# Optimization experiments

Measured on AMD Instinct MI355X. Metric: run time of the kernel, lower is better.

Reference implementation:

```python
import jax, jax.numpy as jnp
import numpy as np


def hadamard(D):
    # Sylvester Hadamard: H[i,j] = (-1)^popcount(i & j), normalized by sqrt(D)
    x = np.arange(D)[:, None] & np.arange(D)[None, :]
    par = np.zeros_like(x)
    for _ in range(int(np.log2(D)) + 1):
        par ^= x & 1
        x >>= 1
    return ((1.0 - 2.0 * par) / np.sqrt(D)).astype(np.float32)


def setup_inputs() -> dict:
    key = jax.random.key(0)
    ks = jax.random.split(key, 6)
    K, M, D, T = 4, 32, 2048, 128
    z = jax.random.normal(ks[0], (K, M, D, T), dtype=jnp.float32)
    d1 = jax.random.normal(ks[1], (D, 1), dtype=jnp.float32)
    d2 = jax.random.normal(ks[2], (D, 1), dtype=jnp.float32)
    d3 = jax.random.normal(ks[3], (D, 1), dtype=jnp.float32)
    b = jax.random.normal(ks[4], (D, 1), dtype=jnp.float32)
    sldj = jax.random.normal(ks[5], (K * M,), dtype=jnp.float32)
    return {"z": z, "d1": d1, "d2": d2, "d3": d3, "b": b,
            "sum_log_det_jacobians": sldj}


def reference(z, d1, d2, d3, b, sum_log_det_jacobians):
    K, M, D, T = z.shape
    H = jnp.asarray(hadamard(D), dtype=z.dtype)
    # A = H @ D3 @ H @ D2 @ H @ D1
    #   H @ diag(d)  == H * d.T (scale columns)
    #   diag(d) @ X  == d * X   (scale rows)
    A = H @ (d3 * (H @ (d2 * (H * d1[:, 0][None, :]))))
    # apply: tensordot(A, z, [[1],[2]]) then transpose to (K,M,D,T), add bias
    z_out = jnp.einsum('de,kmet->kmdt', A, z) + b[None, None, :, :]
    # log|det A| = sum_i log|d1_i| + log|d2_i| + log|d3_i|  (H is orthogonal)
    log_det_A = (jnp.sum(jnp.log(jnp.abs(d1)))
                 + jnp.sum(jnp.log(jnp.abs(d2)))
                 + jnp.sum(jnp.log(jnp.abs(d3))))
    sldj = sum_log_det_jacobians + log_det_A * jnp.ones((K * M,), dtype=z.dtype)
    return z_out, sldj
```

## Files before the change

### kernel.cpp

```cpp
#include <hip/hip_runtime.h>
#include <math.h>

#define D_DIM 2048
#define T_DIM 128
#define TT 16

__device__ __forceinline__ int sw1(int x) { return x ^ ((x >> 5) & 1); }
__device__ __forceinline__ int sw2(int x) { return x ^ ((x >> 4) & 1); }

#define BFLY(MM)                                              \
    _Pragma("unroll")                                         \
    for (int i_ = 0; i_ < 64; ++i_) {                         \
        if ((i_ & (MM)) == 0) {                               \
            float a_ = v[i_], b_ = v[i_ | (MM)];              \
            v[i_] = a_ + b_;                                  \
            v[i_ | (MM)] = a_ - b_;                           \
        }                                                     \
    }

__global__ __launch_bounds__(512, 2)
void fwht_apply_kernel(const float* __restrict__ z,
                       const float* __restrict__ d1,
                       const float* __restrict__ d2,
                       const float* __restrict__ d3,
                       const float* __restrict__ bvec,
                       const float* __restrict__ sldj_in,
                       float* __restrict__ out) {
    __shared__ float lds[1024 * TT];
    const int tid = threadIdx.x;

    if (blockIdx.x == 1024) {
        float acc = 0.0f;
        for (int i = tid; i < D_DIM; i += 512)
            acc += logf(fabsf(d1[i])) + logf(fabsf(d2[i])) + logf(fabsf(d3[i]));
        lds[tid] = acc;
        __syncthreads();
        #pragma unroll
        for (int sft = 256; sft > 0; sft >>= 1) {
            if (tid < sft) lds[tid] += lds[tid + sft];
            __syncthreads();
        }
        if (tid < 128)
            out[(size_t)4 * 32 * 2048 * 128 + tid] = sldj_in[tid] + lds[0];
        return;
    }

    const int r   = tid >> 4;
    const int tt  = tid & 15;
    const int bid = blockIdx.x;
    const int km  = bid >> 3;
    const int t0  = (bid & 7) << 4;
    const float s = 0.022097086912079608f;

    const float* zslab = z + ((size_t)km << 18) + t0;
    const int wid  = tid >> 6;
    const int lane = tid & 63;
    const int q    = lane >> 2;
    const int c    = lane & 3;

    float v[64];

    #pragma unroll
    for (int h = 0; h < 2; ++h) {
        #pragma unroll
        for (int i = 0; i < 8; ++i) {
            const int n = (wid << 3) | i;
            const int e = (n << 5) | (h << 4) | q;
            float4 tmp = *(const float4*)(zslab + (size_t)e * T_DIM + (c << 2));
            ((float4*)lds)[(n << 6) + (q << 2) + c] = tmp;
        }
        __syncthreads();
        if (((r >> 4) & 1) == h) {
            #pragma unroll
            for (int j = 0; j < 64; ++j) {
                const int e = (j << 5) | r;
                v[j] = lds[(((r & 15) | (j << 4)) << 4) + tt] * (d1[e] * s);
            }
        }
        __syncthreads();
    }

    BFLY(1) BFLY(2) BFLY(4) BFLY(8) BFLY(16) BFLY(32)

    #pragma unroll
    for (int j = 0; j < 32; ++j)
        lds[sw1((j << 5) | r) * TT + tt] = v[j];
    __syncthreads();
    #pragma unroll
    for (int j = 0; j < 32; ++j)
        v[j] = lds[sw1(j | (r << 5)) * TT + tt];
    __syncthreads();
    #pragma unroll
    for (int j = 32; j < 64; ++j)
        lds[sw1(((j & 31) << 5) | r) * TT + tt] = v[j];
    __syncthreads();
    #pragma unroll
    for (int j = 32; j < 64; ++j)
        v[j] = lds[sw1((j & 31) | (r << 5)) * TT + tt];
    __syncthreads();

    BFLY(1) BFLY(2) BFLY(4) BFLY(8) BFLY(16)
    {
        const float4* q0 = (const float4*)(d2 + (r << 5));
        const float4* q1 = (const float4*)(d2 + 1024 + (r << 5));
        #pragma unroll
        for (int qq = 0; qq < 8; ++qq) {
            float4 a = q0[qq];
            v[4*qq+0] *= a.x * s; v[4*qq+1] *= a.y * s;
            v[4*qq+2] *= a.z * s; v[4*qq+3] *= a.w * s;
            float4 cc = q1[qq];
            v[32+4*qq+0] *= cc.x * s; v[32+4*qq+1] *= cc.y * s;
            v[32+4*qq+2] *= cc.z * s; v[32+4*qq+3] *= cc.w * s;
        }
    }
    BFLY(1) BFLY(2) BFLY(4) BFLY(8) BFLY(16) BFLY(32)

    #pragma unroll
    for (int j = 0; j < 64; j += 2)
        lds[sw2(((j >> 1) & 15) | (r << 4) | ((j >> 5) << 9)) * TT + tt] = v[j];
    __syncthreads();
    #pragma unroll
    for (int j = 0; j < 64; j += 2)
        v[j] = lds[sw2((((j >> 1) & 31) << 4) | (r & 15) | ((r >> 4) << 9)) * TT + tt];
    __syncthreads();
    #pragma unroll
    for (int j = 1; j < 64; j += 2)
        lds[sw2(((j >> 1) & 15) | (r << 4) | ((j >> 5) << 9)) * TT + tt] = v[j];
    __syncthreads();
    #pragma unroll
    for (int j = 1; j < 64; j += 2)
        v[j] = lds[sw2((((j >> 1) & 31) << 4) | (r & 15) | ((r >> 4) << 9)) * TT + tt];
    __syncthreads();

    BFLY(2) BFLY(4) BFLY(8) BFLY(16) BFLY(32)
    {
        const int eRest = ((r & 15) << 1) | ((r >> 4) << 10);
        #pragma unroll
        for (int m = 0; m < 32; ++m) {
            float2 a = *(const float2*)(d3 + ((m << 5) | eRest));
            v[2*m]   *= a.x * s;
            v[2*m+1] *= a.y * s;
        }
    }
    BFLY(2) BFLY(4) BFLY(8) BFLY(16) BFLY(32) BFLY(1)

    #pragma unroll
    for (int j = 0; j < 64; j += 2)
        lds[sw2((((j >> 1) & 31) << 4) | (r & 15) | ((r >> 4) << 9)) * TT + tt] = v[j];
    __syncthreads();
    #pragma unroll
    for (int j = 0; j < 64; j += 2)
        v[j] = lds[sw2(((j >> 1) & 15) | (r << 4) | ((j >> 5) << 9)) * TT + tt];
    __syncthreads();
    #pragma unroll
    for (int j = 1; j < 64; j += 2)
        lds[sw2((((j >> 1) & 31) << 4) | (r & 15) | ((r >> 4) << 9)) * TT + tt] = v[j];
    __syncthreads();
    #pragma unroll
    for (int j = 1; j < 64; j += 2)
        v[j] = lds[sw2(((j >> 1) & 15) | (r << 4) | ((j >> 5) << 9)) * TT + tt];

    BFLY(2) BFLY(4) BFLY(8) BFLY(16) BFLY(32)

    float* ob = out + ((size_t)km << 18) + t0 + tt;
    {
        const float4* q0 = (const float4*)(bvec + (r << 5));
        const float4* q1 = (const float4*)(bvec + 1024 + (r << 5));
        #pragma unroll
        for (int qq = 0; qq < 8; ++qq) {
            float4 a = q0[qq];
            const int e0 = (r << 5) + 4*qq;
            ob[(size_t)(e0+0) * T_DIM] = v[4*qq+0] + a.x;
            ob[(size_t)(e0+1) * T_DIM] = v[4*qq+1] + a.y;
            ob[(size_t)(e0+2) * T_DIM] = v[4*qq+2] + a.z;
            ob[(size_t)(e0+3) * T_DIM] = v[4*qq+3] + a.w;
            float4 cc = q1[qq];
            const int e1 = 1024 + (r << 5) + 4*qq;
            ob[(size_t)(e1+0) * T_DIM] = v[32+4*qq+0] + cc.x;
            ob[(size_t)(e1+1) * T_DIM] = v[32+4*qq+1] + cc.y;
            ob[(size_t)(e1+2) * T_DIM] = v[32+4*qq+2] + cc.z;
            ob[(size_t)(e1+3) * T_DIM] = v[32+4*qq+3] + cc.w;
        }
    }
}

extern "C" void kernel_launch(void* const* d_in, const int* in_sizes, int n_in,
                              void* d_out, int out_size, void* d_ws, size_t ws_size,
                              hipStream_t stream) {
    const float* z    = (const float*)d_in[0];
    const float* d1   = (const float*)d_in[1];
    const float* d2   = (const float*)d_in[2];
    const float* d3   = (const float*)d_in[3];
    const float* bvec = (const float*)d_in[4];
    const float* sldj = (const float*)d_in[5];
    float* out = (float*)d_out;

    fwht_apply_kernel<<<1025, 512, 0, stream>>>(z, d1, d2, d3, bvec, sldj, out);
}
```

Measured before the change: 303.4 us.

## Halve block to 256 threads with 8-column tiles and two passes per block

New measurement: 835.5 us. +175.4%, slower.

```diff
diff --git a/kernel.cpp b/kernel.cpp
--- a/kernel.cpp
+++ b/kernel.cpp
@@ -3,10 +3,10 @@
 
 #define D_DIM 2048
 #define T_DIM 128
-#define TT 16
-
-__device__ __forceinline__ int sw1(int x) { return x ^ ((x >> 5) & 1); }
-__device__ __forceinline__ int sw2(int x) { return x ^ ((x >> 4) & 1); }
+#define TT 8
+
+__device__ __forceinline__ int sw1(int x) { return x ^ ((x >> 5) & 3); }
+__device__ __forceinline__ int sw2(int x) { return x ^ ((x >> 4) & 3); }
 
 #define BFLY(MM)                                              \
     _Pragma("unroll")                                         \
@@ -18,7 +18,7 @@
         }                                                     \
     }
 
-__global__ __launch_bounds__(512, 2)
+__global__ __launch_bounds__(256, 4)
 void fwht_apply_kernel(const float* __restrict__ z,
                        const float* __restrict__ d1,
                        const float* __restrict__ d2,
@@ -31,12 +31,12 @@
 
     if (blockIdx.x == 1024) {
         float acc = 0.0f;
-        for (int i = tid; i < D_DIM; i += 512)
+        for (int i = tid; i < D_DIM; i += 256)
             acc += logf(fabsf(d1[i])) + logf(fabsf(d2[i])) + logf(fabsf(d3[i]));
         lds[tid] = acc;
         __syncthreads();
         #pragma unroll
-        for (int sft = 256; sft > 0; sft >>= 1) {
+        for (int sft = 128; sft > 0; sft >>= 1) {
             if (tid < sft) lds[tid] += lds[tid + sft];
             __syncthreads();
         }
@@ -45,141 +45,147 @@
         return;
     }
 
-    const int r   = tid >> 4;
-    const int tt  = tid & 15;
+    const int r   = tid >> 3;
+    const int tt  = tid & 7;
     const int bid = blockIdx.x;
-    const int km  = bid >> 3;
-    const int t0  = (bid & 7) << 4;
+    const int km  = bid & 127;
+    const int p0  = bid >> 7;
     const float s = 0.022097086912079608f;
 
-    const float* zslab = z + ((size_t)km << 18) + t0;
     const int wid  = tid >> 6;
     const int lane = tid & 63;
-    const int q    = lane >> 2;
-    const int c    = lane & 3;
-
-    float v[64];
-
-    #pragma unroll
-    for (int h = 0; h < 2; ++h) {
-        #pragma unroll
-        for (int i = 0; i < 8; ++i) {
-            const int n = (wid << 3) | i;
-            const int e = (n << 5) | (h << 4) | q;
-            float4 tmp = *(const float4*)(zslab + (size_t)e * T_DIM + (c << 2));
-            ((float4*)lds)[(n << 6) + (q << 2) + c] = tmp;
-        }
-        __syncthreads();
-        if (((r >> 4) & 1) == h) {
-            #pragma unroll
-            for (int j = 0; j < 64; ++j) {
-                const int e = (j << 5) | r;
-                v[j] = lds[(((r & 15) | (j << 4)) << 4) + tt] * (d1[e] * s);
-            }
-        }
-        __syncthreads();
-    }
-
-    BFLY(1) BFLY(2) BFLY(4) BFLY(8) BFLY(16) BFLY(32)
-
-    #pragma unroll
-    for (int j = 0; j < 32; ++j)
-        lds[sw1((j << 5) | r) * TT + tt] = v[j];
-    __syncthreads();
-    #pragma unroll
-    for (int j = 0; j < 32; ++j)
-        v[j] = lds[sw1(j | (r << 5)) * TT + tt];
-    __syncthreads();
-    #pragma unroll
-    for (int j = 32; j < 64; ++j)
-        lds[sw1(((j & 31) << 5) | r) * TT + tt] = v[j];
-    __syncthreads();
-    #pragma unroll
-    for (int j = 32; j < 64; ++j)
-        v[j] = lds[sw1((j & 31) | (r << 5)) * TT + tt];
-    __syncthreads();
-
-    BFLY(1) BFLY(2) BFLY(4) BFLY(8) BFLY(16)
-    {
-        const float4* q0 = (const float4*)(d2 + (r << 5));
-        const float4* q1 = (const float4*)(d2 + 1024 + (r << 5));
-        #pragma unroll
-        for (int qq = 0; qq < 8; ++qq) {
-            float4 a = q0[qq];
-            v[4*qq+0] *= a.x * s; v[4*qq+1] *= a.y * s;
-            v[4*qq+2] *= a.z * s; v[4*qq+3] *= a.w * s;
-            float4 cc = q1[qq];
-            v[32+4*qq+0] *= cc.x * s; v[32+4*qq+1] *= cc.y * s;
-            v[32+4*qq+2] *= cc.z * s; v[32+4*qq+3] *= cc.w * s;
-        }
-    }
-    BFLY(1) BFLY(2) BFLY(4) BFLY(8) BFLY(16) BFLY(32)
-
-    #pragma unroll
-    for (int j = 0; j < 64; j += 2)
-        lds[sw2(((j >> 1) & 15) | (r << 4) | ((j >> 5) << 9)) * TT + tt] = v[j];
-    __syncthreads();
-    #pragma unroll
-    for (int j = 0; j < 64; j += 2)
-        v[j] = lds[sw2((((j >> 1) & 31) << 4) | (r & 15) | ((r >> 4) << 9)) * TT + tt];
-    __syncthreads();
-    #pragma unroll
-    for (int j = 1; j < 64; j += 2)
-        lds[sw2(((j >> 1) & 15) | (r << 4) | ((j >> 5) << 9)) * TT + tt] = v[j];
-    __syncthreads();
-    #pragma unroll
-    for (int j = 1; j < 64; j += 2)
-        v[j] = lds[sw2((((j >> 1) & 31) << 4) | (r & 15) | ((r >> 4) << 9)) * TT + tt];
-    __syncthreads();
-
-    BFLY(2) BFLY(4) BFLY(8) BFLY(16) BFLY(32)
-    {
-        const int eRest = ((r & 15) << 1) | ((r >> 4) << 10);
-        #pragma unroll
-        for (int m = 0; m < 32; ++m) {
-            float2 a = *(const float2*)(d3 + ((m << 5) | eRest));
-            v[2*m]   *= a.x * s;
-            v[2*m+1] *= a.y * s;
-        }
-    }
-    BFLY(2) BFLY(4) BFLY(8) BFLY(16) BFLY(32) BFLY(1)
-
-    #pragma unroll
-    for (int j = 0; j < 64; j += 2)
-        lds[sw2((((j >> 1) & 31) << 4) | (r & 15) | ((r >> 4) << 9)) * TT + tt] = v[j];
-    __syncthreads();
-    #pragma unroll
-    for (int j = 0; j < 64; j += 2)
-        v[j] = lds[sw2(((j >> 1) & 15) | (r << 4) | ((j >> 5) << 9)) * TT + tt];
-    __syncthreads();
-    #pragma unroll
-    for (int j = 1; j < 64; j += 2)
-        lds[sw2((((j >> 1) & 31) << 4) | (r & 15) | ((r >> 4) << 9)) * TT + tt] = v[j];
-    __syncthreads();
-    #pragma unroll
-    for (int j = 1; j < 64; j += 2)
-        v[j] = lds[sw2(((j >> 1) & 15) | (r << 4) | ((j >> 5) << 9)) * TT + tt];
-
-    BFLY(2) BFLY(4) BFLY(8) BFLY(16) BFLY(32)
-
-    float* ob = out + ((size_t)km << 18) + t0 + tt;
-    {
-        const float4* q0 = (const float4*)(bvec + (r << 5));
-        const float4* q1 = (const float4*)(bvec + 1024 + (r << 5));
-        #pragma unroll
-        for (int qq = 0; qq < 8; ++qq) {
-            float4 a = q0[qq];
-            const int e0 = (r << 5) + 4*qq;
-            ob[(size_t)(e0+0) * T_DIM] = v[4*qq+0] + a.x;
-            ob[(size_t)(e0+1) * T_DIM] = v[4*qq+1] + a.y;
-            ob[(size_t)(e0+2) * T_DIM] = v[4*qq+2] + a.z;
-            ob[(size_t)(e0+3) * T_DIM] = v[4*qq+3] + a.w;
-            float4 cc = q1[qq];
-            const int e1 = 1024 + (r << 5) + 4*qq;
-            ob[(size_t)(e1+0) * T_DIM] = v[32+4*qq+0] + cc.x;
-            ob[(size_t)(e1+1) * T_DIM] = v[32+4*qq+1] + cc.y;
-            ob[(size_t)(e1+2) * T_DIM] = v[32+4*qq+2] + cc.z;
-            ob[(size_t)(e1+3) * T_DIM] = v[32+4*qq+3] + cc.w;
+    const int q    = (lane >> 1) & 15;
+    const int c    = lane & 1;
+    const int nl   = lane >> 5;
+
+    #pragma unroll 1
+    for (int p = 0; p < 2; ++p) {
+        const int t0 = (p0 << 4) | (p << 3);
+        const float* zslab = z + ((size_t)km << 18) + t0;
+        float v[64];
+        __syncthreads();
+
+        #pragma unroll
+        for (int h = 0; h < 2; ++h) {
+            #pragma unroll
+            for (int i = 0; i < 8; ++i) {
+                const int n = (wid << 4) | (i << 1) | nl;
+                const int e = (n << 5) | (h << 4) | q;
+                float4 tmp = *(const float4*)(zslab + (size_t)e * T_DIM + (c << 2));
+                ((float4*)lds)[(n << 5) + (q << 1) + c] = tmp;
+            }
+            __syncthreads();
+            if (((r >> 4) & 1) == h) {
+                #pragma unroll
+                for (int j = 0; j < 64; ++j) {
+                    const int e = (j << 5) | r;
+                    v[j] = lds[(j << 7) + ((r & 15) << 3) + tt] * (d1[e] * s);
+                }
+            }
+            __syncthreads();
+        }
+
+        BFLY(1) BFLY(2) BFLY(4) BFLY(8) BFLY(16) BFLY(32)
+
+        #pragma unroll
+        for (int j = 0; j < 32; ++j)
+            lds[(sw1((j << 5) | r) << 3) + tt] = v[j];
+        __syncthreads();
+        #pragma unroll
+        for (int j = 0; j < 32; ++j)
+            v[j] = lds[(sw1(j | (r << 5)) << 3) + tt];
+        __syncthreads();
+        #pragma unroll
+        for (int j = 32; j < 64; ++j)
+            lds[(sw1(((j & 31) << 5) | r) << 3) + tt] = v[j];
+        __syncthreads();
+        #pragma unroll
+        for (int j = 32; j < 64; ++j)
+            v[j] = lds[(sw1((j & 31) | (r << 5)) << 3) + tt];
+        __syncthreads();
+
+        BFLY(1) BFLY(2) BFLY(4) BFLY(8) BFLY(16)
+        {
+            const float4* q0 = (const float4*)(d2 + (r << 5));
+            const float4* q1 = (const float4*)(d2 + 1024 + (r << 5));
+            #pragma unroll
+            for (int qq = 0; qq < 8; ++qq) {
+                float4 a = q0[qq];
+                v[4*qq+0] *= a.x * s; v[4*qq+1] *= a.y * s;
+                v[4*qq+2] *= a.z * s; v[4*qq+3] *= a.w * s;
+                float4 cc = q1[qq];
+                v[32+4*qq+0] *= cc.x * s; v[32+4*qq+1] *= cc.y * s;
+                v[32+4*qq+2] *= cc.z * s; v[32+4*qq+3] *= cc.w * s;
+            }
+        }
+        BFLY(1) BFLY(2) BFLY(4) BFLY(8) BFLY(16) BFLY(32)
+
+        #pragma unroll
+        for (int j = 0; j < 64; j += 2)
+            lds[(sw2(((j >> 1) & 15) | (r << 4) | ((j >> 5) << 9)) << 3) + tt] = v[j];
+        __syncthreads();
+        #pragma unroll
+        for (int j = 0; j < 64; j += 2)
+            v[j] = lds[(sw2((((j >> 1) & 31) << 4) | (r & 15) | ((r >> 4) << 9)) << 3) + tt];
+        __syncthreads();
+        #pragma unroll
+        for (int j = 1; j < 64; j += 2)
+            lds[(sw2(((j >> 1) & 15) | (r << 4) | ((j >> 5) << 9)) << 3) + tt] = v[j];
+        __syncthreads();
+        #pragma unroll
+        for (int j = 1; j < 64; j += 2)
+            v[j] = lds[(sw2((((j >> 1) & 31) << 4) | (r & 15) | ((r >> 4) << 9)) << 3) + tt];
+        __syncthreads();
+
+        BFLY(2) BFLY(4) BFLY(8) BFLY(16) BFLY(32)
+        {
+            const int eRest = ((r & 15) << 1) | ((r >> 4) << 10);
+            #pragma unroll
+            for (int m = 0; m < 32; ++m) {
+                float2 a = *(const float2*)(d3 + ((m << 5) | eRest));
+                v[2*m]   *= a.x * s;
+                v[2*m+1] *= a.y * s;
+            }
+        }
+        BFLY(2) BFLY(4) BFLY(8) BFLY(16) BFLY(32) BFLY(1)
+
+        #pragma unroll
+        for (int j = 0; j < 64; j += 2)
+            lds[(sw2((((j >> 1) & 31) << 4) | (r & 15) | ((r >> 4) << 9)) << 3) + tt] = v[j];
+        __syncthreads();
+        #pragma unroll
+        for (int j = 0; j < 64; j += 2)
+            v[j] = lds[(sw2(((j >> 1) & 15) | (r << 4) | ((j >> 5) << 9)) << 3) + tt];
+        __syncthreads();
+        #pragma unroll
+        for (int j = 1; j < 64; j += 2)
+            lds[(sw2((((j >> 1) & 31) << 4) | (r & 15) | ((r >> 4) << 9)) << 3) + tt] = v[j];
+        __syncthreads();
+        #pragma unroll
+        for (int j = 1; j < 64; j += 2)
+            v[j] = lds[(sw2(((j >> 1) & 15) | (r << 4) | ((j >> 5) << 9)) << 3) + tt];
+
+        BFLY(2) BFLY(4) BFLY(8) BFLY(16) BFLY(32)
+
+        float* ob = out + ((size_t)km << 18) + t0 + tt;
+        {
+            const float4* q0 = (const float4*)(bvec + (r << 5));
+            const float4* q1 = (const float4*)(bvec + 1024 + (r << 5));
+            #pragma unroll
+            for (int qq = 0; qq < 8; ++qq) {
+                float4 a = q0[qq];
+                const int e0 = (r << 5) + 4*qq;
+                ob[(size_t)(e0+0) * T_DIM] = v[4*qq+0] + a.x;
+                ob[(size_t)(e0+1) * T_DIM] = v[4*qq+1] + a.y;
+                ob[(size_t)(e0+2) * T_DIM] = v[4*qq+2] + a.z;
+                ob[(size_t)(e0+3) * T_DIM] = v[4*qq+3] + a.w;
+                float4 cc = q1[qq];
+                const int e1 = 1024 + (r << 5) + 4*qq;
+                ob[(size_t)(e1+0) * T_DIM] = v[32+4*qq+0] + cc.x;
+                ob[(size_t)(e1+1) * T_DIM] = v[32+4*qq+1] + cc.y;
+                ob[(size_t)(e1+2) * T_DIM] = v[32+4*qq+2] + cc.z;
+                ob[(size_t)(e1+3) * T_DIM] = v[32+4*qq+3] + cc.w;
+            }
         }
     }
 }
@@ -195,5 +201,5 @@
     const float* sldj = (const float*)d_in[5];
     float* out = (float*)d_out;
 
-    fwht_apply_kernel<<<1025, 512, 0, stream>>>(z, d1, d2, d3, bvec, sldj, out);
+    fwht_apply_kernel<<<1025, 256, 0, stream>>>(z, d1, d2, d3, bvec, sldj, out);
 }
```

## Halve LDS footprint with quarter-sized transposes and register-prefetched loads

Applied to the files above, without the earlier changes.

Measured after the change: 335.3 us. +10.5%, slower.

```diff
diff --git a/kernel.cpp b/kernel.cpp
--- a/kernel.cpp
+++ b/kernel.cpp
@@ -3,10 +3,10 @@
 
 #define D_DIM 2048
 #define T_DIM 128
-#define TT 16
-
-__device__ __forceinline__ int sw1(int x) { return x ^ ((x >> 5) & 1); }
-__device__ __forceinline__ int sw2(int x) { return x ^ ((x >> 4) & 1); }
+
+__device__ __forceinline__ int W(int row, int tt) {
+    return ((row ^ ((row >> 4) & 1)) << 4) | tt;
+}
 
 #define BFLY(MM)                                              \
     _Pragma("unroll")                                         \
@@ -26,7 +26,7 @@
                        const float* __restrict__ bvec,
                        const float* __restrict__ sldj_in,
                        float* __restrict__ out) {
-    __shared__ float lds[1024 * TT];
+    __shared__ float lds[512 * 16];
     const int tid = threadIdx.x;
 
     if (blockIdx.x == 1024) {
@@ -52,29 +52,43 @@
     const int t0  = (bid & 7) << 4;
     const float s = 0.022097086912079608f;
 
-    const float* zslab = z + ((size_t)km << 18) + t0;
-    const int wid  = tid >> 6;
+    const int wv   = tid >> 6;
     const int lane = tid & 63;
     const int q    = lane >> 2;
     const int c    = lane & 3;
 
+    const float* zb = z + ((size_t)km << 18) + t0 + (c << 2);
+
     float v[64];
 
-    #pragma unroll
-    for (int h = 0; h < 2; ++h) {
-        #pragma unroll
-        for (int i = 0; i < 8; ++i) {
-            const int n = (wid << 3) | i;
-            const int e = (n << 5) | (h << 4) | q;
-            float4 tmp = *(const float4*)(zslab + (size_t)e * T_DIM + (c << 2));
-            ((float4*)lds)[(n << 6) + (q << 2) + c] = tmp;
+    float4 pf[4];
+    #pragma unroll
+    for (int i = 0; i < 4; ++i) {
+        const int row = (wv << 6) | (i << 4) | q;
+        const int e   = ((row >> 3) << 5) | (row & 7);
+        pf[i] = *(const float4*)(zb + (size_t)e * T_DIM);
+    }
+    #pragma unroll
+    for (int h = 0; h < 4; ++h) {
+        #pragma unroll
+        for (int i = 0; i < 4; ++i) {
+            const int row = (wv << 6) | (i << 4) | q;
+            *(float4*)&lds[W(row, c << 2)] = pf[i];
+        }
+        if (h < 3) {
+            #pragma unroll
+            for (int i = 0; i < 4; ++i) {
+                const int row = (wv << 6) | (i << 4) | q;
+                const int e   = ((row >> 3) << 5) | ((h + 1) << 3) | (row & 7);
+                pf[i] = *(const float4*)(zb + (size_t)e * T_DIM);
+            }
         }
         __syncthreads();
-        if (((r >> 4) & 1) == h) {
+        if ((r >> 3) == h) {
             #pragma unroll
             for (int j = 0; j < 64; ++j) {
                 const int e = (j << 5) | r;
-                v[j] = lds[(((r & 15) | (j << 4)) << 4) + tt] * (d1[e] * s);
+                v[j] = lds[W((j << 3) | (r & 7), tt)] * (d1[e] * s);
             }
         }
         __syncthreads();
@@ -83,21 +97,25 @@
     BFLY(1) BFLY(2) BFLY(4) BFLY(8) BFLY(16) BFLY(32)
 
     #pragma unroll
-    for (int j = 0; j < 32; ++j)
-        lds[sw1((j << 5) | r) * TT + tt] = v[j];
-    __syncthreads();
-    #pragma unroll
-    for (int j = 0; j < 32; ++j)
-        v[j] = lds[sw1(j | (r << 5)) * TT + tt];
-    __syncthreads();
-    #pragma unroll
-    for (int j = 32; j < 64; ++j)
-        lds[sw1(((j & 31) << 5) | r) * TT + tt] = v[j];
-    __syncthreads();
-    #pragma unroll
-    for (int j = 32; j < 64; ++j)
-        v[j] = lds[sw1((j & 31) | (r << 5)) * TT + tt];
-    __syncthreads();
+    for (int h1 = 0; h1 < 2; ++h1) {
+        #pragma unroll
+        for (int h2 = 0; h2 < 2; ++h2) {
+            if ((r & 1) == h2) {
+                #pragma unroll
+                for (int jj = 0; jj < 32; ++jj) {
+                    const int j = (h1 << 5) | jj;
+                    lds[W((jj << 4) | (r >> 1), tt)] = v[j];
+                }
+            }
+            __syncthreads();
+            #pragma unroll
+            for (int jj = 0; jj < 16; ++jj) {
+                const int j = (h1 << 5) | (jj << 1) | h2;
+                v[j] = lds[W((r << 4) | jj, tt)];
+            }
+            __syncthreads();
+        }
+    }
 
     BFLY(1) BFLY(2) BFLY(4) BFLY(8) BFLY(16)
     {
@@ -116,21 +134,25 @@
     BFLY(1) BFLY(2) BFLY(4) BFLY(8) BFLY(16) BFLY(32)
 
     #pragma unroll
-    for (int j = 0; j < 64; j += 2)
-        lds[sw2(((j >> 1) & 15) | (r << 4) | ((j >> 5) << 9)) * TT + tt] = v[j];
-    __syncthreads();
-    #pragma unroll
-    for (int j = 0; j < 64; j += 2)
-        v[j] = lds[sw2((((j >> 1) & 31) << 4) | (r & 15) | ((r >> 4) << 9)) * TT + tt];
-    __syncthreads();
-    #pragma unroll
-    for (int j = 1; j < 64; j += 2)
-        lds[sw2(((j >> 1) & 15) | (r << 4) | ((j >> 5) << 9)) * TT + tt] = v[j];
-    __syncthreads();
-    #pragma unroll
-    for (int j = 1; j < 64; j += 2)
-        v[j] = lds[sw2((((j >> 1) & 31) << 4) | (r & 15) | ((r >> 4) << 9)) * TT + tt];
-    __syncthreads();
+    for (int h1 = 0; h1 < 2; ++h1) {
+        #pragma unroll
+        for (int h2 = 0; h2 < 2; ++h2) {
+            #pragma unroll
+            for (int jj = 0; jj < 16; ++jj) {
+                const int j = (h1 << 5) | (jj << 1) | h2;
+                lds[W((r << 4) | jj, tt)] = v[j];
+            }
+            __syncthreads();
+            if ((r >> 4) == h1) {
+                #pragma unroll
+                for (int jj = 0; jj < 32; ++jj) {
+                    const int j = (jj << 1) | h2;
+                    v[j] = lds[W((jj << 4) | (r & 15), tt)];
+                }
+            }
+            __syncthreads();
+        }
+    }
 
     BFLY(2) BFLY(4) BFLY(8) BFLY(16) BFLY(32)
     {
@@ -145,20 +167,25 @@
     BFLY(2) BFLY(4) BFLY(8) BFLY(16) BFLY(32) BFLY(1)
 
     #pragma unroll
-    for (int j = 0; j < 64; j += 2)
-        lds[sw2((((j >> 1) & 31) << 4) | (r & 15) | ((r >> 4) << 9)) * TT + tt] = v[j];
-    __syncthreads();
-    #pragma unroll
-    for (int j = 0; j < 64; j += 2)
-        v[j] = lds[sw2(((j >> 1) & 15) | (r << 4) | ((j >> 5) << 9)) * TT + tt];
-    __syncthreads();
-    #pragma unroll
-    for (int j = 1; j < 64; j += 2)
-        lds[sw2((((j >> 1) & 31) << 4) | (r & 15) | ((r >> 4) << 9)) * TT + tt] = v[j];
-    __syncthreads();
-    #pragma unroll
-    for (int j = 1; j < 64; j += 2)
-        v[j] = lds[sw2(((j >> 1) & 15) | (r << 4) | ((j >> 5) << 9)) * TT + tt];
+    for (int h1 = 0; h1 < 2; ++h1) {
+        #pragma unroll
+        for (int h2 = 0; h2 < 2; ++h2) {
+            if ((r >> 4) == h1) {
+                #pragma unroll
+                for (int jj = 0; jj < 32; ++jj) {
+                    const int j = (jj << 1) | h2;
+                    lds[W((jj << 4) | (r & 15), tt)] = v[j];
+                }
+            }
+            __syncthreads();
+            #pragma unroll
+            for (int jj = 0; jj < 16; ++jj) {
+                const int j = (h1 << 5) | (jj << 1) | h2;
+                v[j] = lds[W((r << 4) | jj, tt)];
+            }
+            if (!(h1 == 1 && h2 == 1)) __syncthreads();
+        }
+    }
 
     BFLY(2) BFLY(4) BFLY(8) BFLY(16) BFLY(32)
 
```

## Make blocks persistent over four tiles with async global-to-LDS double-buffered prefetch

Applied to the files above, without the earlier changes.

Result: slower. 314.7 us (+3.7%).

```diff
diff --git a/kernel.cpp b/kernel.cpp
--- a/kernel.cpp
+++ b/kernel.cpp
@@ -4,6 +4,9 @@
 #define D_DIM 2048
 #define T_DIM 128
 #define TT 16
+
+typedef __attribute__((address_space(1))) const unsigned int gu32;
+typedef __attribute__((address_space(3))) unsigned int su32;
 
 __device__ __forceinline__ int sw1(int x) { return x ^ ((x >> 5) & 1); }
 __device__ __forceinline__ int sw2(int x) { return x ^ ((x >> 4) & 1); }
@@ -18,6 +21,13 @@
         }                                                     \
     }
 
+__device__ __forceinline__ void barx() {
+    asm volatile("s_waitcnt lgkmcnt(0)" ::: "memory");
+    __builtin_amdgcn_s_barrier();
+    asm volatile("" ::: "memory");
+}
+#define VWAIT(N) asm volatile("s_waitcnt vmcnt(" #N ")" ::: "memory")
+
 __global__ __launch_bounds__(512, 2)
 void fwht_apply_kernel(const float* __restrict__ z,
                        const float* __restrict__ d1,
@@ -26,160 +36,188 @@
                        const float* __restrict__ bvec,
                        const float* __restrict__ sldj_in,
                        float* __restrict__ out) {
-    __shared__ float lds[1024 * TT];
+    extern __shared__ float sh[];
+    float* buf0 = sh;
+    float* buf1 = sh + 16384;
+    float* d1l  = sh + 32768;
+    float* d2l  = sh + 34816;
+    float* d3l  = sh + 36864;
+    float* bl   = sh + 38912;
     const int tid = threadIdx.x;
 
-    if (blockIdx.x == 1024) {
+    if (blockIdx.x == 256) {
         float acc = 0.0f;
         for (int i = tid; i < D_DIM; i += 512)
             acc += logf(fabsf(d1[i])) + logf(fabsf(d2[i])) + logf(fabsf(d3[i]));
-        lds[tid] = acc;
+        sh[tid] = acc;
         __syncthreads();
         #pragma unroll
         for (int sft = 256; sft > 0; sft >>= 1) {
-            if (tid < sft) lds[tid] += lds[tid + sft];
+            if (tid < sft) sh[tid] += sh[tid + sft];
             __syncthreads();
         }
         if (tid < 128)
-            out[(size_t)4 * 32 * 2048 * 128 + tid] = sldj_in[tid] + lds[0];
+            out[(size_t)4 * 32 * 2048 * 128 + tid] = sldj_in[tid] + sh[0];
         return;
     }
 
-    const int r   = tid >> 4;
-    const int tt  = tid & 15;
-    const int bid = blockIdx.x;
-    const int km  = bid >> 3;
-    const int t0  = (bid & 7) << 4;
-    const float s = 0.022097086912079608f;
-
-    const float* zslab = z + ((size_t)km << 18) + t0;
+    const int r    = tid >> 4;
+    const int tt   = tid & 15;
+    const int b    = blockIdx.x;
     const int wid  = tid >> 6;
     const int lane = tid & 63;
     const int q    = lane >> 2;
     const int c    = lane & 3;
-
-    float v[64];
-
-    #pragma unroll
-    for (int h = 0; h < 2; ++h) {
+    const float s  = 0.022097086912079608f;
+
+    for (int k = tid; k < D_DIM; k += 512) {
+        d1l[k] = d1[k] * s;
+        d2l[k] = d2[k] * s;
+        d3l[k] = d3[k] * s;
+        bl[k]  = bvec[k];
+    }
+
+    auto issue = [&](float* buf, int tau, int h) {
+        const float* zs = z + ((size_t)(tau >> 3) << 18) + ((tau & 7) << 4) + (c << 2);
         #pragma unroll
         for (int i = 0; i < 8; ++i) {
             const int n = (wid << 3) | i;
             const int e = (n << 5) | (h << 4) | q;
-            float4 tmp = *(const float4*)(zslab + (size_t)e * T_DIM + (c << 2));
-            ((float4*)lds)[(n << 6) + (q << 2) + c] = tmp;
-        }
-        __syncthreads();
-        if (((r >> 4) & 1) == h) {
-            #pragma unroll
-            for (int j = 0; j < 64; ++j) {
-                const int e = (j << 5) | r;
-                v[j] = lds[(((r & 15) | (j << 4)) << 4) + tt] * (d1[e] * s);
+            __builtin_amdgcn_global_load_lds((gu32*)(zs + (size_t)e * T_DIM),
+                                             (su32*)(buf + (n << 8)), 16, 0, 0);
+        }
+    };
+
+    issue(buf0, b << 2, 0);
+
+    #pragma unroll 1
+    for (int ti = 0; ti < 4; ++ti) {
+        const int tau = (b << 2) | ti;
+        float v[64];
+
+        barx();
+        issue(buf1, tau, 1);
+        VWAIT(8);
+        barx();
+        if (r < 16) {
+            #pragma unroll
+            for (int j = 0; j < 64; ++j)
+                v[j] = buf0[(((j << 4) | (r & 15)) << 4) + tt] * d1l[(j << 5) | r];
+        }
+        barx();
+        if (ti < 3) { issue(buf0, tau + 1, 0); VWAIT(8); }
+        else        { VWAIT(0); }
+        barx();
+        if (r >= 16) {
+            #pragma unroll
+            for (int j = 0; j < 64; ++j)
+                v[j] = buf1[(((j << 4) | (r & 15)) << 4) + tt] * d1l[(j << 5) | r];
+        }
+        barx();
+
+        float* tl = buf1;
+
+        BFLY(1) BFLY(2) BFLY(4) BFLY(8) BFLY(16) BFLY(32)
+
+        #pragma unroll
+        for (int j = 0; j < 32; ++j)
+            tl[sw1((j << 5) | r) * TT + tt] = v[j];
+        barx();
+        #pragma unroll
+        for (int j = 0; j < 32; ++j)
+            v[j] = tl[sw1(j | (r << 5)) * TT + tt];
+        barx();
+        #pragma unroll
+        for (int j = 32; j < 64; ++j)
+            tl[sw1(((j & 31) << 5) | r) * TT + tt] = v[j];
+        barx();
+        #pragma unroll
+        for (int j = 32; j < 64; ++j)
+            v[j] = tl[sw1((j & 31) | (r << 5)) * TT + tt];
+        barx();
+
+        BFLY(1) BFLY(2) BFLY(4) BFLY(8) BFLY(16)
+        {
+            const float4* q0 = (const float4*)(d2l + (r << 5));
+            const float4* q1 = (const float4*)(d2l + 1024 + (r << 5));
+            #pragma unroll
+            for (int qq = 0; qq < 8; ++qq) {
+                float4 a = q0[qq];
+                v[4*qq+0] *= a.x; v[4*qq+1] *= a.y;
+                v[4*qq+2] *= a.z; v[4*qq+3] *= a.w;
+                float4 cc = q1[qq];
+                v[32+4*qq+0] *= cc.x; v[32+4*qq+1] *= cc.y;
+                v[32+4*qq+2] *= cc.z; v[32+4*qq+3] *= cc.w;
             }
         }
-        __syncthreads();
-    }
-
-    BFLY(1) BFLY(2) BFLY(4) BFLY(8) BFLY(16) BFLY(32)
-
-    #pragma unroll
-    for (int j = 0; j < 32; ++j)
-        lds[sw1((j << 5) | r) * TT + tt] = v[j];
-    __syncthreads();
-    #pragma unroll
-    for (int j = 0; j < 32; ++j)
-        v[j] = lds[sw1(j | (r << 5)) * TT + tt];
-    __syncthreads();
-    #pragma unroll
-    for (int j = 32; j < 64; ++j)
-        lds[sw1(((j & 31) << 5) | r) * TT + tt] = v[j];
-    __syncthreads();
-    #pragma unroll
-    for (int j = 32; j < 64; ++j)
-        v[j] = lds[sw1((j & 31) | (r << 5)) * TT + tt];
-    __syncthreads();
-
-    BFLY(1) BFLY(2) BFLY(4) BFLY(8) BFLY(16)
-    {
-        const float4* q0 = (const float4*)(d2 + (r << 5));
-        const float4* q1 = (const float4*)(d2 + 1024 + (r << 5));
-        #pragma unroll
-        for (int qq = 0; qq < 8; ++qq) {
-            float4 a = q0[qq];
-            v[4*qq+0] *= a.x * s; v[4*qq+1] *= a.y * s;
-            v[4*qq+2] *= a.z * s; v[4*qq+3] *= a.w * s;
-            float4 cc = q1[qq];
-            v[32+4*qq+0] *= cc.x * s; v[32+4*qq+1] *= cc.y * s;
-            v[32+4*qq+2] *= cc.z * s; v[32+4*qq+3] *= cc.w * s;
-        }
-    }
-    BFLY(1) BFLY(2) BFLY(4) BFLY(8) BFLY(16) BFLY(32)
-
-    #pragma unroll
-    for (int j = 0; j < 64; j += 2)
-        lds[sw2(((j >> 1) & 15) | (r << 4) | ((j >> 5) << 9)) * TT + tt] = v[j];
-    __syncthreads();
-    #pragma unroll
-    for (int j = 0; j < 64; j += 2)
-        v[j] = lds[sw2((((j >> 1) & 31) << 4) | (r & 15) | ((r >> 4) << 9)) * TT + tt];
-    __syncthreads();
-    #pragma unroll
-    for (int j = 1; j < 64; j += 2)
-        lds[sw2(((j >> 1) & 15) | (r << 4) | ((j >> 5) << 9)) * TT + tt] = v[j];
-    __syncthreads();
-    #pragma unroll
-    for (int j = 1; j < 64; j += 2)
-        v[j] = lds[sw2((((j >> 1) & 31) << 4) | (r & 15) | ((r >> 4) << 9)) * TT + tt];
-    __syncthreads();
-
-    BFLY(2) BFLY(4) BFLY(8) BFLY(16) BFLY(32)
-    {
-        const int eRest = ((r & 15) << 1) | ((r >> 4) << 10);
-        #pragma unroll
-        for (int m = 0; m < 32; ++m) {
-            float2 a = *(const float2*)(d3 + ((m << 5) | eRest));
-            v[2*m]   *= a.x * s;
-            v[2*m+1] *= a.y * s;
-        }
-    }
-    BFLY(2) BFLY(4) BFLY(8) BFLY(16) BFLY(32) BFLY(1)
-
-    #pragma unroll
-    for (int j = 0; j < 64; j += 2)
-        lds[sw2((((j >> 1) & 31) << 4) | (r & 15) | ((r >> 4) << 9)) * TT + tt] = v[j];
-    __syncthreads();
-    #pragma unroll
-    for (int j = 0; j < 64; j += 2)
-        v[j] = lds[sw2(((j >> 1) & 15) | (r << 4) | ((j >> 5) << 9)) * TT + tt];
-    __syncthreads();
-    #pragma unroll
-    for (int j = 1; j < 64; j += 2)
-        lds[sw2((((j >> 1) & 31) << 4) | (r & 15) | ((r >> 4) << 9)) * TT + tt] = v[j];
-    __syncthreads();
-    #pragma unroll
-    for (int j = 1; j < 64; j += 2)
-        v[j] = lds[sw2(((j >> 1) & 15) | (r << 4) | ((j >> 5) << 9)) * TT + tt];
-
-    BFLY(2) BFLY(4) BFLY(8) BFLY(16) BFLY(32)
-
-    float* ob = out + ((size_t)km << 18) + t0 + tt;
-    {
-        const float4* q0 = (const float4*)(bvec + (r << 5));
-        const float4* q1 = (const float4*)(bvec + 1024 + (r << 5));
-        #pragma unroll
-        for (int qq = 0; qq < 8; ++qq) {
-            float4 a = q0[qq];
-            const int e0 = (r << 5) + 4*qq;
-            ob[(size_t)(e0+0) * T_DIM] = v[4*qq+0] + a.x;
-            ob[(size_t)(e0+1) * T_DIM] = v[4*qq+1] + a.y;
-            ob[(size_t)(e0+2) * T_DIM] = v[4*qq+2] + a.z;
-            ob[(size_t)(e0+3) * T_DIM] = v[4*qq+3] + a.w;
-            float4 cc = q1[qq];
-            const int e1 = 1024 + (r << 5) + 4*qq;
-            ob[(size_t)(e1+0) * T_DIM] = v[32+4*qq+0] + cc.x;
-            ob[(size_t)(e1+1) * T_DIM] = v[32+4*qq+1] + cc.y;
-            ob[(size_t)(e1+2) * T_DIM] = v[32+4*qq+2] + cc.z;
-            ob[(size_t)(e1+3) * T_DIM] = v[32+4*qq+3] + cc.w;
+        BFLY(1) BFLY(2) BFLY(4) BFLY(8) BFLY(16) BFLY(32)
+
+        #pragma unroll
+        for (int j = 0; j < 64; j += 2)
+            tl[sw2(((j >> 1) & 15) | (r << 4) | ((j >> 5) << 9)) * TT + tt] = v[j];
+        barx();
+        #pragma unroll
+        for (int j = 0; j < 64; j += 2)
+            v[j] = tl[sw2((((j >> 1) & 31) << 4) | (r & 15) | ((r >> 4) << 9)) * TT + tt];
+        barx();
+        #pragma unroll
+        for (int j = 1; j < 64; j += 2)
+            tl[sw2(((j >> 1) & 15) | (r << 4) | ((j >> 5) << 9)) * TT + tt] = v[j];
+        barx();
+        #pragma unroll
+        for (int j = 1; j < 64; j += 2)
+            v[j] = tl[sw2((((j >> 1) & 31) << 4) | (r & 15) | ((r >> 4) << 9)) * TT + tt];
+        barx();
+
+        BFLY(2) BFLY(4) BFLY(8) BFLY(16) BFLY(32)
+        {
+            const int eRest = ((r & 15) << 1) | ((r >> 4) << 10);
+            #pragma unroll
+            for (int m = 0; m < 32; ++m) {
+                float2 a = *(const float2*)(d3l + ((m << 5) | eRest));
+                v[2*m]   *= a.x;
+                v[2*m+1] *= a.y;
+            }
+        }
+        BFLY(2) BFLY(4) BFLY(8) BFLY(16) BFLY(32) BFLY(1)
+
+        #pragma unroll
+        for (int j = 0; j < 64; j += 2)
+            tl[sw2((((j >> 1) & 31) << 4) | (r & 15) | ((r >> 4) << 9)) * TT + tt] = v[j];
+        barx();
+        #pragma unroll
+        for (int j = 0; j < 64; j += 2)
+            v[j] = tl[sw2(((j >> 1) & 15) | (r << 4) | ((j >> 5) << 9)) * TT + tt];
+        barx();
+        #pragma unroll
+        for (int j = 1; j < 64; j += 2)
+            tl[sw2((((j >> 1) & 31) << 4) | (r & 15) | ((r >> 4) << 9)) * TT + tt] = v[j];
+        barx();
+        #pragma unroll
+        for (int j = 1; j < 64; j += 2)
+            v[j] = tl[sw2(((j >> 1) & 15) | (r << 4) | ((j >> 5) << 9)) * TT + tt];
+
+        BFLY(2) BFLY(4) BFLY(8) BFLY(16) BFLY(32)
+
+        float* ob = out + ((size_t)(tau >> 3) << 18) + ((tau & 7) << 4) + tt;
+        {
+            const float4* q0 = (const float4*)(bl + (r << 5));
+            const float4* q1 = (const float4*)(bl + 1024 + (r << 5));
+            #pragma unroll
+            for (int qq = 0; qq < 8; ++qq) {
+                float4 a = q0[qq];
+                const int e0 = (r << 5) + 4*qq;
+                ob[(size_t)(e0+0) * T_DIM] = v[4*qq+0] + a.x;
+                ob[(size_t)(e0+1) * T_DIM] = v[4*qq+1] + a.y;
+                ob[(size_t)(e0+2) * T_DIM] = v[4*qq+2] + a.z;
+                ob[(size_t)(e0+3) * T_DIM] = v[4*qq+3] + a.w;
+                float4 cc = q1[qq];
+                const int e1 = 1024 + (r << 5) + 4*qq;
+                ob[(size_t)(e1+0) * T_DIM] = v[32+4*qq+0] + cc.x;
+                ob[(size_t)(e1+1) * T_DIM] = v[32+4*qq+1] + cc.y;
+                ob[(size_t)(e1+2) * T_DIM] = v[32+4*qq+2] + cc.z;
+                ob[(size_t)(e1+3) * T_DIM] = v[32+4*qq+3] + cc.w;
+            }
         }
     }
 }
@@ -195,5 +233,8 @@
     const float* sldj = (const float*)d_in[5];
     float* out = (float*)d_out;
 
-    fwht_apply_kernel<<<1025, 512, 0, stream>>>(z, d1, d2, d3, bvec, sldj, out);
+    hipFuncSetAttribute((const void*)fwht_apply_kernel,
+                        hipFuncAttributeMaxDynamicSharedMemorySize, 163840);
+
+    fwht_apply_kernel<<<257, 512, 163840, stream>>>(z, d1, d2, d3, bvec, sldj, out);
 }
```
